# Kernel tuning notes

Hardware: AMD Instinct MI355X
Metric: run time of the kernel (lower is better)

The kernel has to match this reference:

```python
import jax, jax.numpy as jnp
import numpy as np

B, T, E, H, DK, FF = 8, 2048, 64, 8, 8, 256
EPS = 1e-5


def _ln(x, g, b):
    m = jnp.mean(x, axis=-1, keepdims=True)
    v = jnp.mean((x - m) ** 2, axis=-1, keepdims=True)
    return (x - m) * jax.lax.rsqrt(v + EPS) * g + b


def setup_inputs() -> dict:
    key = jax.random.key(0)
    ks = jax.random.split(key, 16)
    s = 0.05
    f32 = jnp.float32
    return {
        "x": jax.random.normal(ks[0], (B, T, E), f32),
        "Wq": jax.random.normal(ks[1], (E, E), f32) * s,
        "bq": jnp.zeros((E,), f32),
        "Wk": jax.random.normal(ks[2], (E, E), f32) * s,
        "bk": jnp.zeros((E,), f32),
        "Wv": jax.random.normal(ks[3], (E, E), f32) * s,
        "bv": jnp.zeros((E,), f32),
        "Wo": jax.random.normal(ks[4], (E, E), f32) * s,
        "bo": jnp.zeros((E,), f32),
        "theta_attn": jax.random.uniform(ks[5], (), f32, 0.0, 2.0 * np.pi),
        "theta_ffn": jax.random.uniform(ks[6], (), f32, 0.0, 2.0 * np.pi),
        "W1": jax.random.normal(ks[7], (FF, E), f32) * s,
        "b1": jnp.zeros((FF,), f32),
        "W2": jax.random.normal(ks[8], (E, FF), f32) * s,
        "b2": jnp.zeros((E,), f32),
        "g1": jnp.ones((E,), f32),
        "be1": jnp.zeros((E,), f32),
        "g2": jnp.ones((E,), f32),
        "be2": jnp.zeros((E,), f32),
    }


def _forward(x, Wq, bq, Wk, bk, Wv, bv, Wo, bo, theta_attn, theta_ffn,
             W1, b1, W2, b2, g1, be1, g2, be2):
    def split(h):  # [B,T,E] -> [B,H,T,DK]
        return h.reshape(B, T, H, DK).transpose(0, 2, 1, 3)

    q = split(x @ Wq.T + bq)
    k = split(x @ Wk.T + bk)
    v = split(x @ Wv.T + bv)
    # per-head quantum circuit: RX(x) then shared RX(theta) -> <Z> = cos(x + theta)
    q = jnp.cos(q + theta_attn)
    k = jnp.cos(k + theta_attn)
    v = jnp.cos(v + theta_attn)
    scores = jnp.einsum('bhtd,bhsd->bhts', q, k) / np.float32(np.sqrt(DK))
    scores = jax.nn.softmax(scores, axis=-1)
    attn = jnp.einsum('bhts,bhsd->bhtd', scores, v)
    attn = attn.transpose(0, 2, 1, 3).reshape(B, T, E) @ Wo.T + bo
    x1 = _ln(x + attn, g1, be1)
    # FFN quantum circuit: RX(x) then shared RY(theta) -> <Z> = cos(x)*cos(theta)
    qout = jnp.cos(x1) * jnp.cos(theta_ffn)
    f = jax.nn.relu(qout @ W1.T + b1) @ W2.T + b2
    return _ln(x1 + f, g2, be2)


def reference(x, Wq, bq, Wk, bk, Wv, bv, Wo, bo, theta_attn, theta_ffn,
              W1, b1, W2, b2, g1, be1, g2, be2):
    return _forward(x, Wq, bq, Wk, bk, Wv, bv, Wo, bo, theta_attn, theta_ffn,
                    W1, b1, W2, b2, g1, be1, g2, be2)
```

## Files before the change

### kernel.cpp

```cpp
#include <hip/hip_runtime.h>
#include <hip/hip_bf16.h>

#define B_ 8
#define T_ 2048
#define NROWS 16384

typedef __attribute__((ext_vector_type(16))) float f32x16;
typedef __attribute__((ext_vector_type(8))) short short8;
typedef __fp16 half2_t __attribute__((ext_vector_type(2)));
typedef __fp16 half8_t __attribute__((ext_vector_type(8)));

__device__ __forceinline__ unsigned int pkrtz(float a, float b) {
    half2_t h = __builtin_amdgcn_cvt_pkrtz(a, b);
    return __builtin_bit_cast(unsigned int, h);
}
__device__ __forceinline__ unsigned int pkbf(float a, float b) {
    return __builtin_amdgcn_perm(__float_as_uint(b), __float_as_uint(a), 0x07060302u);
}
__device__ __forceinline__ float dot2(unsigned int a, unsigned int b, float c) {
    return __builtin_amdgcn_fdot2(__builtin_bit_cast(half2_t, a),
                                  __builtin_bit_cast(half2_t, b), c, false);
}
__device__ __forceinline__ float fast_exp2(float x) {
#if __has_builtin(__builtin_amdgcn_exp2f)
    return __builtin_amdgcn_exp2f(x);
#else
    return exp2f(x);
#endif
}

__global__ __launch_bounds__(512, 2) void qkv_kernel(
    const float* __restrict__ x,
    const float* __restrict__ Wq, const float* __restrict__ bq,
    const float* __restrict__ Wk, const float* __restrict__ bk,
    const float* __restrict__ Wv, const float* __restrict__ bv,
    const float* __restrict__ theta_attn,
    unsigned short* __restrict__ qb, unsigned short* __restrict__ kbuf,
    unsigned short* __restrict__ vbuf)
{
    __shared__ unsigned int xpk[32 * 66];
    __shared__ unsigned int wpk[32 * 196];
    __shared__ unsigned int outs[6144];
    const int tid = threadIdx.x;
    const int n0 = blockIdx.x * 64;

    #pragma unroll
    for (int t = 0; t < 2; t++) {
        int fi = tid + t * 512;
        float4 v = ((const float4*)(x + (size_t)n0 * 64))[fi];
        int r = fi >> 4, k0 = (fi & 15) * 4;
        xpk[(k0 >> 1) * 66 + r] = pkrtz(v.x, v.y);
        xpk[((k0 >> 1) + 1) * 66 + r] = pkrtz(v.z, v.w);
    }
    const float* Wm[3] = {Wq, Wk, Wv};
    #pragma unroll
    for (int t = 0; t < 6; t++) {
        int fi = tid + t * 512;
        int m = fi >> 10, j = (fi >> 4) & 63, k0 = (fi & 15) * 4;
        float4 v = ((const float4*)Wm[m])[fi & 1023];
        wpk[(k0 >> 1) * 196 + m * 64 + j] = pkrtz(v.x, v.y);
        wpk[((k0 >> 1) + 1) * 196 + m * 64 + j] = pkrtz(v.z, v.w);
    }
    __syncthreads();

    const int r0 = (tid & 31) * 2;
    const int c0 = (tid >> 5) * 12;
    float acc[2][12] = {};
    #pragma unroll 8
    for (int kp = 0; kp < 32; kp++) {
        uint2 a = *(const uint2*)&xpk[kp * 66 + r0];
        uint4 b0 = *(const uint4*)&wpk[kp * 196 + c0];
        uint4 b1 = *(const uint4*)&wpk[kp * 196 + c0 + 4];
        uint4 b2 = *(const uint4*)&wpk[kp * 196 + c0 + 8];
        unsigned int bb[12] = {b0.x, b0.y, b0.z, b0.w,
                               b1.x, b1.y, b1.z, b1.w,
                               b2.x, b2.y, b2.z, b2.w};
        #pragma unroll
        for (int j = 0; j < 12; j++) {
            acc[0][j] = dot2(a.x, bb[j], acc[0][j]);
            acc[1][j] = dot2(a.y, bb[j], acc[1][j]);
        }
    }

    {
        const float th = *theta_attn;
        const float QS = 0.51006980f;
        const float* biasp[3] = {bq, bk, bv};
        float bcol[12];
        #pragma unroll
        for (int j = 0; j < 12; j++) {
            int c = c0 + j;
            bcol[j] = biasp[c >> 6][c & 63];
        }
        #pragma unroll
        for (int i = 0; i < 2; i++) {
            float vals[12];
            #pragma unroll
            for (int j = 0; j < 12; j++) {
                float v = __cosf(acc[i][j] + bcol[j] + th);
                vals[j] = ((c0 + j) >> 6) == 0 ? v * QS : v;
            }
            int row = r0 + i;
            #pragma unroll
            for (int t = 0; t < 6; t++) {
                int c = c0 + 2 * t;
                outs[(c >> 3) * 256 + row * 4 + ((c & 7) >> 1)] = pkbf(vals[2*t], vals[2*t+1]);
            }
        }
    }
    __syncthreads();

    unsigned short* outp3[3] = {qb, kbuf, vbuf};
    #pragma unroll
    for (int t = 0; t < 3; t++) {
        int fi = tid + t * 512;
        int bh = fi >> 6, r2 = fi & 63;
        int m = bh >> 3, hI = bh & 7;
        uint4 v = *(const uint4*)&outs[4 * fi];
        int n = n0 + r2;
        unsigned short* dst = outp3[m] +
            ((size_t)((n >> 11) * 8 + hI) * 2048 + (n & 2047)) * 8;
        *(uint4*)dst = v;
    }
}

__global__ __launch_bounds__(256, 4) void attn_kernel(
    const unsigned short* __restrict__ qb,
    const unsigned short* __restrict__ kbuf,
    const unsigned short* __restrict__ vbuf,
    float* __restrict__ attn)
{
    __shared__ __align__(16) unsigned short Ks[1024 * 8];
    __shared__ __align__(16) unsigned short Vt[9 * 1032];
    const int tid = threadIdx.x;
    const int head = blockIdx.x >> 4;
    const int qblk = blockIdx.x & 15;
    const size_t hoff = (size_t)head * T_ * 8;
    const int wave = tid >> 6, lane = tid & 63;
    const int col = lane & 31, h = lane >> 5;
    const int q0 = qblk * 128 + wave * 32;

    const short8 z8 = {0, 0, 0, 0, 0, 0, 0, 0};
    short8 bqf = z8;
    if (h == 0) bqf = *(const short8*)(qb + hoff + (size_t)(q0 + col) * 8);

    if (tid < 128)
        ((uint4*)(Vt + 8 * 1032))[tid] =
            make_uint4(0x3f803f80u, 0x3f803f80u, 0x3f803f80u, 0x3f803f80u);

    f32x16 oacc = {0.f,0.f,0.f,0.f,0.f,0.f,0.f,0.f,0.f,0.f,0.f,0.f,0.f,0.f,0.f,0.f};
    const f32x16 z16 = {0.f,0.f,0.f,0.f,0.f,0.f,0.f,0.f,0.f,0.f,0.f,0.f,0.f,0.f,0.f,0.f};
    const unsigned short* vbase = &Vt[(col < 9 ? col : 8) * 1032 + 8 * h];
    short8 ak = z8;

    for (int half = 0; half < 2; half++) {
        __syncthreads();
        {
            const uint4* kg = (const uint4*)(kbuf + hoff + (size_t)half * 1024 * 8);
            const uint4* vg = (const uint4*)(vbuf + hoff + (size_t)half * 1024 * 8);
            #pragma unroll
            for (int it = 0; it < 4; it++) {
                int s = tid + it * 256;
                ((uint4*)Ks)[s] = kg[s];
                union { uint4 u; unsigned short us[8]; } cv;
                cv.u = vg[s];
                int sp = (s & ~12) | ((s & 4) << 1) | ((s & 8) >> 1);
                #pragma unroll
                for (int d = 0; d < 8; d++) Vt[d * 1032 + sp] = cv.us[d];
            }
        }
        __syncthreads();

        for (int s0 = 0; s0 < 1024; s0 += 32) {
            if (h == 0) ak = *(const short8*)&Ks[(s0 + col) * 8];
            f32x16 S = __builtin_amdgcn_mfma_f32_32x32x16_bf16(ak, bqf, z16, 0, 0, 0);
            #pragma unroll
            for (int g = 0; g < 2; g++) {
                const int o = g * 8;
                union { unsigned int u[4]; short8 s; } bp;
                bp.u[0] = pkbf(fast_exp2(S[o+0]), fast_exp2(S[o+1]));
                bp.u[1] = pkbf(fast_exp2(S[o+2]), fast_exp2(S[o+3]));
                bp.u[2] = pkbf(fast_exp2(S[o+4]), fast_exp2(S[o+5]));
                bp.u[3] = pkbf(fast_exp2(S[o+6]), fast_exp2(S[o+7]));
                short8 av = *(const short8*)&vbase[s0 + g * 16];
                oacc = __builtin_amdgcn_mfma_f32_32x32x16_bf16(av, bp.s, oacc, 0, 0, 0);
            }
        }
    }

    float tot = oacc[4];
    tot += __shfl_xor(tot, 32);
    const float inv = 1.0f / tot;
    const int bI = head >> 3, hI = head & 7;
    const int q = q0 + col;
    #pragma unroll
    for (int rr = 0; rr < 4; rr++) {
        int d = 4 * h + rr;
        attn[((size_t)bI * 2048 + q) * 64 + hI * 8 + d] = oacc[rr] * inv;
    }
}

__global__ __launch_bounds__(512, 4) void tail_kernel(
    const float* __restrict__ attn, const float* __restrict__ x,
    const float* __restrict__ Wo, const float* __restrict__ bo,
    const float* __restrict__ g1, const float* __restrict__ be1,
    const float* __restrict__ theta_ffn,
    const float* __restrict__ W1, const float* __restrict__ b1,
    const float* __restrict__ W2, const float* __restrict__ b2,
    const float* __restrict__ g2, const float* __restrict__ be2,
    float* __restrict__ outp)
{
    __shared__ unsigned int smem[15744];
    const int tid = threadIdx.x;
    const int lane = tid & 63;
    const int wave = tid >> 6;
    const int h = lane >> 5;
    const int n0 = blockIdx.x * 32;
    const int mrow = tid >> 4;
    const int c0 = (tid & 15) * 4;

    unsigned int* const W1p = smem;
    unsigned int* const W2p = smem;
    unsigned int* const Atp = smem + 9216;
    unsigned int* const qoutp = smem + 9216;
    unsigned int* const Wop = smem + 10368;
    unsigned int* const hrowp = smem + 10368;
    float* const Yf = (float*)(smem + 12672);
    float* const Y2a = (float*)(smem + 14592);
    float* const Y2b = (float*)(smem + 8448);

    const f32x16 z16 = {0.f,0.f,0.f,0.f,0.f,0.f,0.f,0.f,0.f,0.f,0.f,0.f,0.f,0.f,0.f,0.f};

    float4 atv = ((const float4*)(attn + (size_t)n0 * 64))[tid];
    float4 wo0 = ((const float4*)Wo)[tid];
    float4 wo1 = ((const float4*)Wo)[tid + 512];
    float4 xv = *(const float4*)(x + (size_t)(n0 + mrow) * 64 + c0);
    float4 w1r[8];
    #pragma unroll
    for (int t = 0; t < 8; t++) w1r[t] = ((const float4*)W1)[tid + t * 512];

    {
        int r = tid >> 4, k0 = (tid & 15) * 4;
        uint2 a2 = make_uint2(pkrtz(atv.x, atv.y), pkrtz(atv.z, atv.w));
        *(uint2*)&Atp[r * 36 + (k0 >> 1)] = a2;
        uint2 wa = make_uint2(pkrtz(wo0.x, wo0.y), pkrtz(wo0.z, wo0.w));
        *(uint2*)&Wop[r * 36 + (k0 >> 1)] = wa;
        int fi = tid + 512;
        int e1 = fi >> 4, k1 = (fi & 15) * 4;
        uint2 wb = make_uint2(pkrtz(wo1.x, wo1.y), pkrtz(wo1.z, wo1.w));
        *(uint2*)&Wop[e1 * 36 + (k1 >> 1)] = wb;
    }
    __syncthreads();

    #pragma unroll
    for (int t = 0; t < 8; t++) {
        int fi = tid + t * 512;
        int f = fi >> 4, k0 = (fi & 15) * 4;
        uint2 w2 = make_uint2(pkrtz(w1r[t].x, w1r[t].y), pkrtz(w1r[t].z, w1r[t].w));
        *(uint2*)&W1p[f * 36 + (k0 >> 1)] = w2;
    }

    if (wave < 2) {
        const int colo = wave * 32 + (lane & 31);
        f32x16 acc = z16;
        #pragma unroll
        for (int kk = 0; kk < 4; kk++) {
            half8_t a = __builtin_bit_cast(half8_t,
                *(const uint4*)&Atp[(lane & 31) * 36 + kk * 8 + h * 4]);
            half8_t b = __builtin_bit_cast(half8_t,
                *(const uint4*)&Wop[colo * 36 + kk * 8 + h * 4]);
            acc = __builtin_amdgcn_mfma_f32_32x32x16_f16(a, b, acc, 0, 0, 0);
        }
        float bov = bo[colo];
        #pragma unroll
        for (int reg = 0; reg < 16; reg++) {
            int rr = (reg & 3) + 8 * (reg >> 2) + 4 * h;
            Yf[rr * 68 + colo] = acc[reg] + bov;
        }
    }
    __syncthreads();

    float x1v[4];
    {
        float4 yv = *(const float4*)&Yf[mrow * 68 + c0];
        float vv[4] = {xv.x + yv.x, xv.y + yv.y, xv.z + yv.z, xv.w + yv.w};
        float s1 = vv[0] + vv[1] + vv[2] + vv[3];
        float s2 = vv[0]*vv[0] + vv[1]*vv[1] + vv[2]*vv[2] + vv[3]*vv[3];
        #pragma unroll
        for (int m = 1; m <= 8; m <<= 1) {
            s1 += __shfl_xor(s1, m);
            s2 += __shfl_xor(s2, m);
        }
        float mean = s1 * 0.015625f;
        float rstd = rsqrtf(s2 * 0.015625f - mean * mean + 1e-5f);
        float4 g14 = *(const float4*)&g1[c0];
        float4 be14 = *(const float4*)&be1[c0];
        float gg[4] = {g14.x, g14.y, g14.z, g14.w};
        float eb[4] = {be14.x, be14.y, be14.z, be14.w};
        float cth = __cosf(*theta_ffn);
        float qv[4];
        #pragma unroll
        for (int j = 0; j < 4; j++) {
            x1v[j] = (vv[j] - mean) * rstd * gg[j] + eb[j];
            qv[j] = __cosf(x1v[j]) * cth;
        }
        uint2 q2 = make_uint2(pkrtz(qv[0], qv[1]), pkrtz(qv[2], qv[3]));
        *(uint2*)&qoutp[mrow * 36 + (c0 >> 1)] = q2;
    }
    __syncthreads();

    float4 w2r[8];
    #pragma unroll
    for (int t = 0; t < 8; t++) w2r[t] = ((const float4*)W2)[tid + t * 512];

    {
        const int fl = lane & 31;
        f32x16 acc = z16;
        #pragma unroll
        for (int kk = 0; kk < 4; kk++) {
            half8_t a = __builtin_bit_cast(half8_t,
                *(const uint4*)&W1p[(wave * 32 + fl) * 36 + kk * 8 + h * 4]);
            half8_t b = __builtin_bit_cast(half8_t,
                *(const uint4*)&qoutp[fl * 36 + kk * 8 + h * 4]);
            acc = __builtin_amdgcn_mfma_f32_32x32x16_f16(a, b, acc, 0, 0, 0);
        }
        const int row = lane & 31;
        #pragma unroll
        for (int q = 0; q < 4; q++) {
            int fb = wave * 32 + 8 * q + 4 * h;
            float4 b1v = *(const float4*)&b1[fb];
            float h0 = fmaxf(acc[4*q+0] + b1v.x, 0.f);
            float h1 = fmaxf(acc[4*q+1] + b1v.y, 0.f);
            float h2 = fmaxf(acc[4*q+2] + b1v.z, 0.f);
            float h3 = fmaxf(acc[4*q+3] + b1v.w, 0.f);
            uint2 hp = make_uint2(pkrtz(h0, h1), pkrtz(h2, h3));
            *(uint2*)&hrowp[row * 132 + (fb >> 1)] = hp;
        }
    }
    __syncthreads();

    #pragma unroll
    for (int t = 0; t < 8; t++) {
        int fi = tid + t * 512;
        int e = fi >> 6, k0 = (fi & 63) * 4;
        uint2 w2 = make_uint2(pkrtz(w2r[t].x, w2r[t].y), pkrtz(w2r[t].z, w2r[t].w));
        *(uint2*)&W2p[e * 132 + (k0 >> 1)] = w2;
    }
    __syncthreads();

    if (wave < 2) {
        const int colo = wave * 32 + (lane & 31);
        f32x16 acc = z16;
        #pragma unroll
        for (int kk = 0; kk < 16; kk++) {
            half8_t a = __builtin_bit_cast(half8_t,
                *(const uint4*)&hrowp[(lane & 31) * 132 + kk * 8 + h * 4]);
            half8_t b = __builtin_bit_cast(half8_t,
                *(const uint4*)&W2p[colo * 132 + kk * 8 + h * 4]);
            acc = __builtin_amdgcn_mfma_f32_32x32x16_f16(a, b, acc, 0, 0, 0);
        }
        float b2v = b2[colo];
        float* Ydst = wave ? Y2b : Y2a;
        const int cl = lane & 31;
        #pragma unroll
        for (int reg = 0; reg < 16; reg++) {
            int rr = (reg & 3) + 8 * (reg >> 2) + 4 * h;
            Ydst[rr * 36 + cl] = acc[reg] + b2v;
        }
    }
    __syncthreads();

    {
        float4 fv = (c0 < 32) ? *(const float4*)&Y2a[mrow * 36 + c0]
                              : *(const float4*)&Y2b[mrow * 36 + (c0 - 32)];
        float vv[4] = {x1v[0] + fv.x, x1v[1] + fv.y, x1v[2] + fv.z, x1v[3] + fv.w};
        float s1 = vv[0] + vv[1] + vv[2] + vv[3];
        float s2 = vv[0]*vv[0] + vv[1]*vv[1] + vv[2]*vv[2] + vv[3]*vv[3];
        #pragma unroll
        for (int m = 1; m <= 8; m <<= 1) {
            s1 += __shfl_xor(s1, m);
            s2 += __shfl_xor(s2, m);
        }
        float mean = s1 * 0.015625f;
        float rstd = rsqrtf(s2 * 0.015625f - mean * mean + 1e-5f);
        float4 g24 = *(const float4*)&g2[c0];
        float4 be24 = *(const float4*)&be2[c0];
        float4 o;
        o.x = (vv[0] - mean) * rstd * g24.x + be24.x;
        o.y = (vv[1] - mean) * rstd * g24.y + be24.y;
        o.z = (vv[2] - mean) * rstd * g24.z + be24.z;
        o.w = (vv[3] - mean) * rstd * g24.w + be24.w;
        *(float4*)(outp + (size_t)(n0 + mrow) * 64 + c0) = o;
    }
}

extern "C" void kernel_launch(void* const* d_in, const int* in_sizes, int n_in,
                              void* d_out, int out_size, void* d_ws, size_t ws_size,
                              hipStream_t stream)
{
    const float* x   = (const float*)d_in[0];
    const float* Wq  = (const float*)d_in[1];
    const float* bq  = (const float*)d_in[2];
    const float* Wk  = (const float*)d_in[3];
    const float* bk  = (const float*)d_in[4];
    const float* Wv  = (const float*)d_in[5];
    const float* bv  = (const float*)d_in[6];
    const float* Wo  = (const float*)d_in[7];
    const float* bo  = (const float*)d_in[8];
    const float* tha = (const float*)d_in[9];
    const float* thf = (const float*)d_in[10];
    const float* W1  = (const float*)d_in[11];
    const float* b1  = (const float*)d_in[12];
    const float* W2  = (const float*)d_in[13];
    const float* b2  = (const float*)d_in[14];
    const float* g1  = (const float*)d_in[15];
    const float* be1 = (const float*)d_in[16];
    const float* g2  = (const float*)d_in[17];
    const float* be2 = (const float*)d_in[18];

    char* wsb = (char*)d_ws;
    unsigned short* qbp = (unsigned short*)(wsb);
    unsigned short* kbp = (unsigned short*)(wsb + (2u << 20));
    unsigned short* vbp = (unsigned short*)(wsb + (4u << 20));
    float* attn = (float*)(wsb + (6u << 20));

    qkv_kernel<<<256, 512, 0, stream>>>(x, Wq, bq, Wk, bk, Wv, bv, tha, qbp, kbp, vbp);
    attn_kernel<<<1024, 256, 0, stream>>>(qbp, kbp, vbp, attn);
    tail_kernel<<<512, 512, 0, stream>>>(attn, x, Wo, bo, g1, be1, thf,
                                         W1, b1, W2, b2, g2, be2, (float*)d_out);
}
```

Before: 136.8 us.

## Process two query tiles per wave in attention to reuse K/V loads

Each wave in the attention kernel now handles 64 queries (two 32-row MFMA tiles) instead of 32. The grid is halved to 512 blocks, and each block's K/V shared-memory staging and per-step K/V fragment loads are shared across twice as many queries. This cuts staging and LDS read overhead per query and gives the scheduler two independent MFMA/exp chains to interleave. In exchange, register pressure rises (launch bounds lowered to 2) and there are fewer blocks to fill the 256 CUs.

```diff
diff --git a/kernel.cpp b/kernel.cpp
--- a/kernel.cpp
+++ b/kernel.cpp
@@ -124,7 +124,7 @@
     }
 }
 
-__global__ __launch_bounds__(256, 4) void attn_kernel(
+__global__ __launch_bounds__(256, 2) void attn_kernel(
     const unsigned short* __restrict__ qb,
     const unsigned short* __restrict__ kbuf,
     const unsigned short* __restrict__ vbuf,
@@ -133,23 +133,27 @@
     __shared__ __align__(16) unsigned short Ks[1024 * 8];
     __shared__ __align__(16) unsigned short Vt[9 * 1032];
     const int tid = threadIdx.x;
-    const int head = blockIdx.x >> 4;
-    const int qblk = blockIdx.x & 15;
+    const int head = blockIdx.x >> 3;
+    const int qseg = blockIdx.x & 7;
     const size_t hoff = (size_t)head * T_ * 8;
     const int wave = tid >> 6, lane = tid & 63;
     const int col = lane & 31, h = lane >> 5;
-    const int q0 = qblk * 128 + wave * 32;
+    const int q0 = qseg * 256 + wave * 64;
 
     const short8 z8 = {0, 0, 0, 0, 0, 0, 0, 0};
-    short8 bqf = z8;
-    if (h == 0) bqf = *(const short8*)(qb + hoff + (size_t)(q0 + col) * 8);
+    short8 bqf0 = z8, bqf1 = z8;
+    if (h == 0) {
+        bqf0 = *(const short8*)(qb + hoff + (size_t)(q0 + col) * 8);
+        bqf1 = *(const short8*)(qb + hoff + (size_t)(q0 + 32 + col) * 8);
+    }
 
     if (tid < 128)
         ((uint4*)(Vt + 8 * 1032))[tid] =
             make_uint4(0x3f803f80u, 0x3f803f80u, 0x3f803f80u, 0x3f803f80u);
 
-    f32x16 oacc = {0.f,0.f,0.f,0.f,0.f,0.f,0.f,0.f,0.f,0.f,0.f,0.f,0.f,0.f,0.f,0.f};
-    const f32x16 z16 = {0.f,0.f,0.f,0.f,0.f,0.f,0.f,0.f,0.f,0.f,0.f,0.f,0.f,0.f,0.f,0.f};
+    f32x16 oacc0 = {0.f,0.f,0.f,0.f,0.f,0.f,0.f,0.f,0.f,0.f,0.f,0.f,0.f,0.f,0.f,0.f};
+    f32x16 oacc1 = oacc0;
+    const f32x16 z16 = oacc0;
     const unsigned short* vbase = &Vt[(col < 9 ? col : 8) * 1032 + 8 * h];
     short8 ak = z8;
 
@@ -173,30 +177,62 @@
 
         for (int s0 = 0; s0 < 1024; s0 += 32) {
             if (h == 0) ak = *(const short8*)&Ks[(s0 + col) * 8];
-            f32x16 S = __builtin_amdgcn_mfma_f32_32x32x16_bf16(ak, bqf, z16, 0, 0, 0);
-            #pragma unroll
-            for (int g = 0; g < 2; g++) {
-                const int o = g * 8;
+            short8 av0 = *(const short8*)&vbase[s0];
+            short8 av1 = *(const short8*)&vbase[s0 + 16];
+
+            f32x16 S0 = __builtin_amdgcn_mfma_f32_32x32x16_bf16(ak, bqf0, z16, 0, 0, 0);
+            {
                 union { unsigned int u[4]; short8 s; } bp;
-                bp.u[0] = pkbf(fast_exp2(S[o+0]), fast_exp2(S[o+1]));
-                bp.u[1] = pkbf(fast_exp2(S[o+2]), fast_exp2(S[o+3]));
-                bp.u[2] = pkbf(fast_exp2(S[o+4]), fast_exp2(S[o+5]));
-                bp.u[3] = pkbf(fast_exp2(S[o+6]), fast_exp2(S[o+7]));
-                short8 av = *(const short8*)&vbase[s0 + g * 16];
-                oacc = __builtin_amdgcn_mfma_f32_32x32x16_bf16(av, bp.s, oacc, 0, 0, 0);
+                bp.u[0] = pkbf(fast_exp2(S0[0]), fast_exp2(S0[1]));
+                bp.u[1] = pkbf(fast_exp2(S0[2]), fast_exp2(S0[3]));
+                bp.u[2] = pkbf(fast_exp2(S0[4]), fast_exp2(S0[5]));
+                bp.u[3] = pkbf(fast_exp2(S0[6]), fast_exp2(S0[7]));
+                oacc0 = __builtin_amdgcn_mfma_f32_32x32x16_bf16(av0, bp.s, oacc0, 0, 0, 0);
+                bp.u[0] = pkbf(fast_exp2(S0[8]),  fast_exp2(S0[9]));
+                bp.u[1] = pkbf(fast_exp2(S0[10]), fast_exp2(S0[11]));
+                bp.u[2] = pkbf(fast_exp2(S0[12]), fast_exp2(S0[13]));
+                bp.u[3] = pkbf(fast_exp2(S0[14]), fast_exp2(S0[15]));
+                oacc0 = __builtin_amdgcn_mfma_f32_32x32x16_bf16(av1, bp.s, oacc0, 0, 0, 0);
             }
-        }
-    }
-
-    float tot = oacc[4];
-    tot += __shfl_xor(tot, 32);
-    const float inv = 1.0f / tot;
+            f32x16 S1 = __builtin_amdgcn_mfma_f32_32x32x16_bf16(ak, bqf1, z16, 0, 0, 0);
+            {
+                union { unsigned int u[4]; short8 s; } bp;
+                bp.u[0] = pkbf(fast_exp2(S1[0]), fast_exp2(S1[1]));
+                bp.u[1] = pkbf(fast_exp2(S1[2]), fast_exp2(S1[3]));
+                bp.u[2] = pkbf(fast_exp2(S1[4]), fast_exp2(S1[5]));
+                bp.u[3] = pkbf(fast_exp2(S1[6]), fast_exp2(S1[7]));
+                oacc1 = __builtin_amdgcn_mfma_f32_32x32x16_bf16(av0, bp.s, oacc1, 0, 0, 0);
+                bp.u[0] = pkbf(fast_exp2(S1[8]),  fast_exp2(S1[9]));
+                bp.u[1] = pkbf(fast_exp2(S1[10]), fast_exp2(S1[11]));
+                bp.u[2] = pkbf(fast_exp2(S1[12]), fast_exp2(S1[13]));
+                bp.u[3] = pkbf(fast_exp2(S1[14]), fast_exp2(S1[15]));
+                oacc1 = __builtin_amdgcn_mfma_f32_32x32x16_bf16(av1, bp.s, oacc1, 0, 0, 0);
+            }
+        }
+    }
+
     const int bI = head >> 3, hI = head & 7;
-    const int q = q0 + col;
-    #pragma unroll
-    for (int rr = 0; rr < 4; rr++) {
-        int d = 4 * h + rr;
-        attn[((size_t)bI * 2048 + q) * 64 + hI * 8 + d] = oacc[rr] * inv;
+    {
+        float tot = oacc0[4];
+        tot += __shfl_xor(tot, 32);
+        const float inv = 1.0f / tot;
+        const int q = q0 + col;
+        #pragma unroll
+        for (int rr = 0; rr < 4; rr++) {
+            int d = 4 * h + rr;
+            attn[((size_t)bI * 2048 + q) * 64 + hI * 8 + d] = oacc0[rr] * inv;
+        }
+    }
+    {
+        float tot = oacc1[4];
+        tot += __shfl_xor(tot, 32);
+        const float inv = 1.0f / tot;
+        const int q = q0 + 32 + col;
+        #pragma unroll
+        for (int rr = 0; rr < 4; rr++) {
+            int d = 4 * h + rr;
+            attn[((size_t)bI * 2048 + q) * 64 + hI * 8 + d] = oacc1[rr] * inv;
+        }
     }
 }
 
@@ -425,7 +461,7 @@
     float* attn = (float*)(wsb + (6u << 20));
 
     qkv_kernel<<<256, 512, 0, stream>>>(x, Wq, bq, Wk, bk, Wv, bv, tha, qbp, kbp, vbp);
-    attn_kernel<<<1024, 256, 0, stream>>>(qbp, kbp, vbp, attn);
+    attn_kernel<<<512, 256, 0, stream>>>(qbp, kbp, vbp, attn);
     tail_kernel<<<512, 512, 0, stream>>>(attn, x, Wo, bo, g1, be1, thf,
                                          W1, b1, W2, b2, g2, be2, (float*)d_out);
 }
```

Result: slower. 140.1 us (+2.4%).

## Pre-transpose V in QKV kernel and stream it from global in attention

Applied to the files above, without the earlier changes.

The QKV projection kernel now writes V in a transposed, permuted layout, split by head and sequence half, that matches the MFMA operand order. The attention kernel no longer stages and transposes V through LDS with scattered 2-byte stores, a transpose each of the 16 query blocks per head previously repeated. It instead loads V fragments straight from global memory, and the all-ones row used for the softmax denominator moves into registers. The cost is that V is now read from global/L2 inside the inner loop rather than from LDS, and the normalisation constant changes to 2/tot.

```diff
diff --git a/kernel.cpp b/kernel.cpp
--- a/kernel.cpp
+++ b/kernel.cpp
@@ -36,7 +36,7 @@
     const float* __restrict__ Wv, const float* __restrict__ bv,
     const float* __restrict__ theta_attn,
     unsigned short* __restrict__ qb, unsigned short* __restrict__ kbuf,
-    unsigned short* __restrict__ vbuf)
+    unsigned short* __restrict__ vt)
 {
     __shared__ unsigned int xpk[32 * 66];
     __shared__ unsigned int wpk[32 * 196];
@@ -110,28 +110,43 @@
     }
     __syncthreads();
 
-    unsigned short* outp3[3] = {qb, kbuf, vbuf};
-    #pragma unroll
-    for (int t = 0; t < 3; t++) {
+    unsigned short* outp2[2] = {qb, kbuf};
+    #pragma unroll
+    for (int t = 0; t < 2; t++) {
         int fi = tid + t * 512;
         int bh = fi >> 6, r2 = fi & 63;
         int m = bh >> 3, hI = bh & 7;
         uint4 v = *(const uint4*)&outs[4 * fi];
         int n = n0 + r2;
-        unsigned short* dst = outp3[m] +
+        unsigned short* dst = outp2[m] +
             ((size_t)((n >> 11) * 8 + hI) * 2048 + (n & 2047)) * 8;
         *(uint4*)dst = v;
+    }
+    {
+        int head = tid >> 6, d = (tid >> 3) & 7, j = tid & 7;
+        int bh = 16 + head, dw = d >> 1, hb = d & 1;
+        const unsigned short* ob = (const unsigned short*)outs;
+        union { uint4 u; unsigned short us[8]; } pk;
+        #pragma unroll
+        for (int e = 0; e < 8; e++) {
+            int sp = 8 * j + e;
+            int r = (sp & ~12) | ((sp & 4) << 1) | ((sp & 8) >> 1);
+            pk.us[e] = ob[(bh * 256 + r * 4 + dw) * 2 + hb];
+        }
+        int bI = n0 >> 11, tI0 = n0 & 2047;
+        int half = tI0 >> 10, s0v = tI0 & 1023;
+        size_t idx = ((((size_t)(bI * 8 + head) * 2 + half) * 8 + d) * 1024 + s0v + 8 * j);
+        *(uint4*)(vt + idx) = pk.u;
     }
 }
 
 __global__ __launch_bounds__(256, 4) void attn_kernel(
     const unsigned short* __restrict__ qb,
     const unsigned short* __restrict__ kbuf,
-    const unsigned short* __restrict__ vbuf,
+    const unsigned short* __restrict__ vt,
     float* __restrict__ attn)
 {
     __shared__ __align__(16) unsigned short Ks[1024 * 8];
-    __shared__ __align__(16) unsigned short Vt[9 * 1032];
     const int tid = threadIdx.x;
     const int head = blockIdx.x >> 4;
     const int qblk = blockIdx.x & 15;
@@ -141,56 +156,59 @@
     const int q0 = qblk * 128 + wave * 32;
 
     const short8 z8 = {0, 0, 0, 0, 0, 0, 0, 0};
+    union { uint4 u; short8 s; } onesu;
+    onesu.u = make_uint4(0x3f803f80u, 0x3f803f80u, 0x3f803f80u, 0x3f803f80u);
+    const short8 ones8 = onesu.s;
+
     short8 bqf = z8;
     if (h == 0) bqf = *(const short8*)(qb + hoff + (size_t)(q0 + col) * 8);
 
-    if (tid < 128)
-        ((uint4*)(Vt + 8 * 1032))[tid] =
-            make_uint4(0x3f803f80u, 0x3f803f80u, 0x3f803f80u, 0x3f803f80u);
-
     f32x16 oacc = {0.f,0.f,0.f,0.f,0.f,0.f,0.f,0.f,0.f,0.f,0.f,0.f,0.f,0.f,0.f,0.f};
-    const f32x16 z16 = {0.f,0.f,0.f,0.f,0.f,0.f,0.f,0.f,0.f,0.f,0.f,0.f,0.f,0.f,0.f,0.f};
-    const unsigned short* vbase = &Vt[(col < 9 ? col : 8) * 1032 + 8 * h];
+    const f32x16 z16 = oacc;
     short8 ak = z8;
 
     for (int half = 0; half < 2; half++) {
         __syncthreads();
         {
             const uint4* kg = (const uint4*)(kbuf + hoff + (size_t)half * 1024 * 8);
-            const uint4* vg = (const uint4*)(vbuf + hoff + (size_t)half * 1024 * 8);
             #pragma unroll
             for (int it = 0; it < 4; it++) {
                 int s = tid + it * 256;
                 ((uint4*)Ks)[s] = kg[s];
-                union { uint4 u; unsigned short us[8]; } cv;
-                cv.u = vg[s];
-                int sp = (s & ~12) | ((s & 4) << 1) | ((s & 8) >> 1);
-                #pragma unroll
-                for (int d = 0; d < 8; d++) Vt[d * 1032 + sp] = cv.us[d];
             }
         }
         __syncthreads();
 
+        const unsigned short* vrow =
+            vt + (((size_t)head * 2 + half) * 8 + col) * 1024 + 8 * h;
+
         for (int s0 = 0; s0 < 1024; s0 += 32) {
+            short8 av0 = ones8, av1 = ones8;
+            if (col < 8) {
+                av0 = *(const short8*)&vrow[s0];
+                av1 = *(const short8*)&vrow[s0 + 16];
+            }
             if (h == 0) ak = *(const short8*)&Ks[(s0 + col) * 8];
             f32x16 S = __builtin_amdgcn_mfma_f32_32x32x16_bf16(ak, bqf, z16, 0, 0, 0);
-            #pragma unroll
-            for (int g = 0; g < 2; g++) {
-                const int o = g * 8;
+            {
                 union { unsigned int u[4]; short8 s; } bp;
-                bp.u[0] = pkbf(fast_exp2(S[o+0]), fast_exp2(S[o+1]));
-                bp.u[1] = pkbf(fast_exp2(S[o+2]), fast_exp2(S[o+3]));
-                bp.u[2] = pkbf(fast_exp2(S[o+4]), fast_exp2(S[o+5]));
-                bp.u[3] = pkbf(fast_exp2(S[o+6]), fast_exp2(S[o+7]));
-                short8 av = *(const short8*)&vbase[s0 + g * 16];
-                oacc = __builtin_amdgcn_mfma_f32_32x32x16_bf16(av, bp.s, oacc, 0, 0, 0);
+                bp.u[0] = pkbf(fast_exp2(S[0]), fast_exp2(S[1]));
+                bp.u[1] = pkbf(fast_exp2(S[2]), fast_exp2(S[3]));
+                bp.u[2] = pkbf(fast_exp2(S[4]), fast_exp2(S[5]));
+                bp.u[3] = pkbf(fast_exp2(S[6]), fast_exp2(S[7]));
+                oacc = __builtin_amdgcn_mfma_f32_32x32x16_bf16(av0, bp.s, oacc, 0, 0, 0);
+                bp.u[0] = pkbf(fast_exp2(S[8]),  fast_exp2(S[9]));
+                bp.u[1] = pkbf(fast_exp2(S[10]), fast_exp2(S[11]));
+                bp.u[2] = pkbf(fast_exp2(S[12]), fast_exp2(S[13]));
+                bp.u[3] = pkbf(fast_exp2(S[14]), fast_exp2(S[15]));
+                oacc = __builtin_amdgcn_mfma_f32_32x32x16_bf16(av1, bp.s, oacc, 0, 0, 0);
             }
         }
     }
 
     float tot = oacc[4];
     tot += __shfl_xor(tot, 32);
-    const float inv = 1.0f / tot;
+    const float inv = 2.0f / tot;
     const int bI = head >> 3, hI = head & 7;
     const int q = q0 + col;
     #pragma unroll
@@ -421,11 +439,11 @@
     char* wsb = (char*)d_ws;
     unsigned short* qbp = (unsigned short*)(wsb);
     unsigned short* kbp = (unsigned short*)(wsb + (2u << 20));
-    unsigned short* vbp = (unsigned short*)(wsb + (4u << 20));
+    unsigned short* vtp = (unsigned short*)(wsb + (4u << 20));
     float* attn = (float*)(wsb + (6u << 20));
 
-    qkv_kernel<<<256, 512, 0, stream>>>(x, Wq, bq, Wk, bk, Wv, bv, tha, qbp, kbp, vbp);
-    attn_kernel<<<1024, 256, 0, stream>>>(qbp, kbp, vbp, attn);
+    qkv_kernel<<<256, 512, 0, stream>>>(x, Wq, bq, Wk, bk, Wv, bv, tha, qbp, kbp, vtp);
+    attn_kernel<<<1024, 256, 0, stream>>>(qbp, kbp, vtp, attn);
     tail_kernel<<<512, 512, 0, stream>>>(attn, x, Wo, bo, g1, be1, thf,
                                          W1, b1, W2, b2, g2, be2, (float*)d_out);
 }
```

Result: slower. 142.2 us (+3.9%).
